# Kernel optimization log

Measured on AMD Instinct MI355X. Metric: run time of the kernel, lower is better.

The kernel has to match this reference:

```python
import jax, jax.numpy as jnp
import numpy as np


def setup_inputs() -> dict:
    key = jax.random.key(0)
    ks = jax.random.split(key, 8)
    B, C, T, F = 2, 2, 500, 129
    H, D = 16, 100  # hidden_channels, delay
    return {
        "x_mic": jax.random.normal(ks[0], (B, C, T, F), jnp.float32),
        "x_ref": jax.random.normal(ks[1], (B, C, T, F), jnp.float32),
        "w_mic": jax.random.normal(ks[2], (H, C), jnp.float32) * 0.5,
        "b_mic": jax.random.normal(ks[3], (H,), jnp.float32) * 0.1,
        "w_ref": jax.random.normal(ks[4], (H, C), jnp.float32) * 0.5,
        "b_ref": jax.random.normal(ks[5], (H,), jnp.float32) * 0.1,
        "w_conv": jax.random.normal(ks[6], (1, H, 5, 3), jnp.float32) * 0.05,
        "b_conv": jax.random.normal(ks[7], (1,), jnp.float32) * 0.1,
        "delay": D,
    }


def reference(x_mic, x_ref, w_mic, b_mic, w_ref, b_ref, w_conv, b_conv, delay):
    # x_mic, x_ref: (B, C, T, F)
    B, C, T, F = x_mic.shape
    # 1x1 convs == per-(t,f) channel mixing
    Q = jnp.einsum('bctf,hc->bhtf', x_mic, w_mic) + b_mic[None, :, None, None]
    K = jnp.einsum('bctf,hc->bhtf', x_ref, w_ref) + b_ref[None, :, None, None]

    # unfold: zero-pad (delay-1) frames at the start of T, take sliding windows
    # window index d at output frame t maps to K[t - (delay-1) + d]
    idx = jnp.arange(T)[:, None] + jnp.arange(delay)[None, :]  # (T, delay) indices into padded T
    Kp = jnp.pad(K, ((0, 0), (0, 0), (delay - 1, 0), (0, 0)))
    Ku = Kp[:, :, idx, :]  # (B, H, T, delay, F)

    # windowed cross-correlation over frequency
    V = jnp.einsum('bhtf,bhtdf->bhtd', Q, Ku)  # (B, H, T, delay)

    # (5,3) conv, causal pad 4 along T (height), symmetric pad 1 along delay (width)
    V = jax.lax.conv_general_dilated(
        V, w_conv, window_strides=(1, 1), padding=[(4, 0), (1, 1)],
        dimension_numbers=('NCHW', 'OIHW', 'NCHW'))
    V = V + b_conv[None, :, None, None]  # (B, 1, T, delay)

    A = jax.nn.softmax(V[:, 0], axis=-1)  # (B, T, delay) attention over delays

    # unfold raw x_ref the same way and take delay-weighted sum
    Rp = jnp.pad(x_ref, ((0, 0), (0, 0), (delay - 1, 0), (0, 0)))
    Ru = Rp[:, :, idx, :]  # (B, C, T, delay, F)
    y = jnp.einsum('bctdf,btd->bctf', Ru, A)  # (B, C, T, F)
    return y
```

## Files before the change

### kernel.cpp

```cpp
#include <hip/hip_runtime.h>
#include <math.h>

constexpr int NB = 2;
constexpr int NC = 2;
constexpr int NT = 500;
constexpr int NF = 129;
constexpr int NH = 16;
constexpr int ND = 100;

constexpr int NMAP = 9;
constexpr size_t CSTRIDE = (size_t)NT * ND;
constexpr size_t CELEMS  = (size_t)NB * NMAP * CSTRIDE;

typedef _Float16 f16;
typedef _Float16 f16x4 __attribute__((ext_vector_type(4)));
typedef float    f32x4 __attribute__((ext_vector_type(4)));

constexpr int TT    = 16;
constexpr int NTT   = 32;
constexpr int BROWS = 128;
constexpr int LROWS = 176;
constexpr int LSTR  = 148;

__global__ __launch_bounds__(256) void corr_kernel(
    const float* __restrict__ x_mic, const float* __restrict__ x_ref,
    float* __restrict__ C)
{
    __shared__ f16 Lds[LROWS * LSTR];

    const int tid = threadIdx.x;
    const int tt = blockIdx.x & 31;
    const int bj = blockIdx.x >> 5;
    const int j = bj % 3, b = bj / 3;
    const int ts = tt * TT;
    const int US = ts - (ND - 1);

    const float* xr = x_ref + (size_t)b * NC * NT * NF;
    const float* xm = x_mic + (size_t)b * NC * NT * NF;

    const int w = tid >> 6;
    const int l = tid & 63;

    for (int rr = 0; rr < 44; ++rr) {
        const int r = w + 4 * rr;
        f16* row = Lds + r * LSTR;
        float v0 = 0.f, v1 = 0.f, v2 = 0.f;
        if (r < BROWS) {
            const int u = US + r;
            if (u >= 0 && u < NT) {
                if (j < 2) {
                    const float* p = xr + (size_t)j * NT * NF + (size_t)u * NF;
                    v0 = p[l]; v1 = p[l + 64]; if (l == 0) v2 = p[128];
                } else { v0 = 1.f; v1 = 1.f; if (l == 0) v2 = 1.f; }
            }
        } else {
            const int q = r - BROWS;
            const int i = q >> 4;
            const int t = ts + (q & 15);
            if (t < NT) {
                if (i < 2) {
                    const float* p = xm + (size_t)i * NT * NF + (size_t)t * NF;
                    v0 = p[l]; v1 = p[l + 64]; if (l == 0) v2 = p[128];
                } else { v0 = 1.f; v1 = 1.f; if (l == 0) v2 = 1.f; }
            }
        }
        row[l]      = (f16)v0;
        row[l + 64] = (f16)v1;
        if (l < LSTR - 128) row[128 + l] = (l == 0) ? (f16)v2 : (f16)0.f;
    }
    __syncthreads();

    const int lr = l & 15;
    const int lk = l >> 4;
    f32x4 acc[3][2] = {};

    #pragma unroll
    for (int kk = 0; kk < 9; ++kk) {
        const int fo = 16 * kk + 4 * lk;
        f16x4 bf0 = *(const f16x4*)&Lds[(32*w      + lr) * LSTR + fo];
        f16x4 bf1 = *(const f16x4*)&Lds[(32*w + 16 + lr) * LSTR + fo];
        #pragma unroll
        for (int i = 0; i < 3; ++i) {
            f16x4 af = *(const f16x4*)&Lds[(BROWS + 16*i + lr) * LSTR + fo];
            acc[i][0] = __builtin_amdgcn_mfma_f32_16x16x16f16(af, bf0, acc[i][0], 0, 0, 0);
            acc[i][1] = __builtin_amdgcn_mfma_f32_16x16x16f16(af, bf1, acc[i][1], 0, 0, 0);
        }
    }

    #pragma unroll
    for (int i = 0; i < 3; ++i) {
        float* Cb = C + ((size_t)b * NMAP + (i*3 + j)) * CSTRIDE;
        #pragma unroll
        for (int n = 0; n < 2; ++n) {
            const int u_loc = 32*w + 16*n + lr;
            #pragma unroll
            for (int jj = 0; jj < 4; ++jj) {
                const int t_loc = 4*lk + jj;
                const int t_g = ts + t_loc;
                const int d = u_loc - t_loc;
                if (t_g < NT && d >= 0 && d < ND)
                    Cb[(size_t)t_g * ND + d] = acc[i][n][jj];
            }
        }
    }
}

__global__ __launch_bounds__(256) void csy_kernel(
    const float* __restrict__ C, const float* __restrict__ w_conv,
    const float* __restrict__ b_conv,
    const float* __restrict__ w_mic, const float* __restrict__ b_mic,
    const float* __restrict__ w_ref, const float* __restrict__ b_ref,
    const float* __restrict__ x_ref, float* __restrict__ y)
{
    const int t = blockIdx.x % NT;
    const int b = blockIdx.x / NT;
    const int tid = threadIdx.x;

    __shared__ float G[NMAP][15];
    __shared__ float Alds[ND];
    __shared__ float red[4];

    if (tid < NMAP * 15) {
        const int m = tid / 15, tap = tid % 15;
        const int i = m / 3, jj = m % 3;
        float s = 0.f;
        for (int h = 0; h < NH; ++h) {
            const float a  = (i  < 2) ? w_mic[h*NC + i]  : b_mic[h];
            const float bb = (jj < 2) ? w_ref[h*NC + jj] : b_ref[h];
            s += w_conv[h*15 + tap] * a * bb;
        }
        G[m][tap] = s;
    }
    __syncthreads();

    const int d = tid;
    float s = 0.f;
    if (d < ND) {
        const float* Cb = C + (size_t)b * NMAP * CSTRIDE;
        #pragma unroll
        for (int kt = 0; kt < 5; ++kt) {
            const int tp = t - 4 + kt;
            if (tp < 0) continue;
            #pragma unroll
            for (int kd = 0; kd < 3; ++kd) {
                const int dp = d - 1 + kd;
                if (dp < 0 || dp >= ND) continue;
                const float* p = Cb + (size_t)tp * ND + dp;
                const int tap = kt*3 + kd;
                float a2 = 0.f;
                #pragma unroll
                for (int m = 0; m < NMAP; ++m)
                    a2 += G[m][tap] * p[m * CSTRIDE];
                s += a2;
            }
        }
        s += b_conv[0];
    }

    if (tid < 128) {
        float mx = (d < ND) ? s : -3.4e38f;
        #pragma unroll
        for (int o = 32; o > 0; o >>= 1) mx = fmaxf(mx, __shfl_down(mx, o, 64));
        if ((tid & 63) == 0) red[tid >> 6] = mx;
    }
    __syncthreads();
    const float mx = fmaxf(red[0], red[1]);
    const float e = (d < ND) ? __expf(s - mx) : 0.f;
    if (tid < 128) {
        float sm = e;
        #pragma unroll
        for (int o = 32; o > 0; o >>= 1) sm += __shfl_down(sm, o, 64);
        if ((tid & 63) == 0) red[2 + (tid >> 6)] = sm;
    }
    __syncthreads();
    const float inv = 1.f / (red[2] + red[3]);
    if (d < ND) Alds[d] = e * inv;
    __syncthreads();

    const int d0 = (t >= ND - 1) ? 0 : (ND - 1 - t);
    for (int o = tid; o < NC * NF; o += 256) {
        const int c = o / NF, f = o - c * NF;
        const float* X = x_ref + ((size_t)(b*NC + c) * NT + (t + d0 - (ND - 1))) * NF + f;
        float acc = 0.f;
        #pragma unroll 4
        for (int dd = d0; dd < ND; ++dd) {
            acc += Alds[dd] * X[0];
            X += NF;
        }
        y[((size_t)(b*NC + c) * NT + t) * NF + f] = acc;
    }
}

extern "C" void kernel_launch(void* const* d_in, const int* in_sizes, int n_in,
                              void* d_out, int out_size, void* d_ws, size_t ws_size,
                              hipStream_t stream)
{
    const float* x_mic  = (const float*)d_in[0];
    const float* x_ref  = (const float*)d_in[1];
    const float* w_mic  = (const float*)d_in[2];
    const float* b_mic  = (const float*)d_in[3];
    const float* w_ref  = (const float*)d_in[4];
    const float* b_ref  = (const float*)d_in[5];
    const float* w_conv = (const float*)d_in[6];
    const float* b_conv = (const float*)d_in[7];
    float* y = (float*)d_out;

    float* C = (float*)d_ws;

    corr_kernel<<<dim3(NB * 3 * NTT), dim3(256), 0, stream>>>(x_mic, x_ref, C);
    csy_kernel<<<dim3(NB * NT), dim3(256), 0, stream>>>(
        C, w_conv, b_conv, w_mic, b_mic, w_ref, b_ref, x_ref, y);
}
```

Measured before the change: 108.5 us.

## Replace bias correlation maps with per-frame row sums

```diff
diff --git a/kernel.cpp b/kernel.cpp
--- a/kernel.cpp
+++ b/kernel.cpp
@@ -8,9 +8,9 @@
 constexpr int NH = 16;
 constexpr int ND = 100;
 
-constexpr int NMAP = 9;
 constexpr size_t CSTRIDE = (size_t)NT * ND;
-constexpr size_t CELEMS  = (size_t)NB * NMAP * CSTRIDE;
+constexpr size_t C4ELEMS = (size_t)NB * 4 * CSTRIDE;
+constexpr int RSRLEN = 600;
 
 typedef _Float16 f16;
 typedef _Float16 f16x4 __attribute__((ext_vector_type(4)));
@@ -19,19 +19,19 @@
 constexpr int TT    = 16;
 constexpr int NTT   = 32;
 constexpr int BROWS = 128;
-constexpr int LROWS = 176;
+constexpr int LROWS = 160;
 constexpr int LSTR  = 148;
 
 __global__ __launch_bounds__(256) void corr_kernel(
     const float* __restrict__ x_mic, const float* __restrict__ x_ref,
-    float* __restrict__ C)
+    float* __restrict__ C, float* __restrict__ rsm, float* __restrict__ rsr)
 {
     __shared__ f16 Lds[LROWS * LSTR];
 
     const int tid = threadIdx.x;
     const int tt = blockIdx.x & 31;
     const int bj = blockIdx.x >> 5;
-    const int j = bj % 3, b = bj / 3;
+    const int j = bj & 1, b = bj >> 1;
     const int ts = tt * TT;
     const int US = ts - (ND - 1);
 
@@ -41,27 +41,23 @@
     const int w = tid >> 6;
     const int l = tid & 63;
 
-    for (int rr = 0; rr < 44; ++rr) {
+    for (int rr = 0; rr < 40; ++rr) {
         const int r = w + 4 * rr;
         f16* row = Lds + r * LSTR;
         float v0 = 0.f, v1 = 0.f, v2 = 0.f;
         if (r < BROWS) {
             const int u = US + r;
             if (u >= 0 && u < NT) {
-                if (j < 2) {
-                    const float* p = xr + (size_t)j * NT * NF + (size_t)u * NF;
-                    v0 = p[l]; v1 = p[l + 64]; if (l == 0) v2 = p[128];
-                } else { v0 = 1.f; v1 = 1.f; if (l == 0) v2 = 1.f; }
+                const float* p = xr + (size_t)j * NT * NF + (size_t)u * NF;
+                v0 = p[l]; v1 = p[l + 64]; if (l == 0) v2 = p[128];
             }
         } else {
             const int q = r - BROWS;
             const int i = q >> 4;
             const int t = ts + (q & 15);
             if (t < NT) {
-                if (i < 2) {
-                    const float* p = xm + (size_t)i * NT * NF + (size_t)t * NF;
-                    v0 = p[l]; v1 = p[l + 64]; if (l == 0) v2 = p[128];
-                } else { v0 = 1.f; v1 = 1.f; if (l == 0) v2 = 1.f; }
+                const float* p = xm + (size_t)i * NT * NF + (size_t)t * NF;
+                v0 = p[l]; v1 = p[l + 64]; if (l == 0) v2 = p[128];
             }
         }
         row[l]      = (f16)v0;
@@ -72,7 +68,7 @@
 
     const int lr = l & 15;
     const int lk = l >> 4;
-    f32x4 acc[3][2] = {};
+    f32x4 acc[2][2] = {};
 
     #pragma unroll
     for (int kk = 0; kk < 9; ++kk) {
@@ -80,7 +76,7 @@
         f16x4 bf0 = *(const f16x4*)&Lds[(32*w      + lr) * LSTR + fo];
         f16x4 bf1 = *(const f16x4*)&Lds[(32*w + 16 + lr) * LSTR + fo];
         #pragma unroll
-        for (int i = 0; i < 3; ++i) {
+        for (int i = 0; i < 2; ++i) {
             f16x4 af = *(const f16x4*)&Lds[(BROWS + 16*i + lr) * LSTR + fo];
             acc[i][0] = __builtin_amdgcn_mfma_f32_16x16x16f16(af, bf0, acc[i][0], 0, 0, 0);
             acc[i][1] = __builtin_amdgcn_mfma_f32_16x16x16f16(af, bf1, acc[i][1], 0, 0, 0);
@@ -88,8 +84,8 @@
     }
 
     #pragma unroll
-    for (int i = 0; i < 3; ++i) {
-        float* Cb = C + ((size_t)b * NMAP + (i*3 + j)) * CSTRIDE;
+    for (int i = 0; i < 2; ++i) {
+        float* Cb = C + ((size_t)b * 4 + i*2 + j) * CSTRIDE;
         #pragma unroll
         for (int n = 0; n < 2; ++n) {
             const int u_loc = 32*w + 16*n + lr;
@@ -103,10 +99,40 @@
             }
         }
     }
+
+    #pragma unroll
+    for (int k = 0; k < 4; ++k) {
+        const int u = ts + 4*w + k;
+        if (u < NT) {
+            const float* p = xr + (size_t)j * NT * NF + (size_t)u * NF;
+            float v = p[l] + p[l + 64] + ((l == 0) ? p[128] : 0.f);
+            #pragma unroll
+            for (int o = 32; o > 0; o >>= 1) v += __shfl_down(v, o, 64);
+            if (l == 0) rsr[((size_t)b*2 + j) * RSRLEN + 99 + u] = v;
+        }
+    }
+    if (j == 0) {
+        #pragma unroll
+        for (int k = 0; k < 8; ++k) {
+            const int q = 8*w + k;
+            const int i = q >> 4;
+            const int t = ts + (q & 15);
+            if (t < NT) {
+                const float* p = xm + (size_t)i * NT * NF + (size_t)t * NF;
+                float v = p[l] + p[l + 64] + ((l == 0) ? p[128] : 0.f);
+                #pragma unroll
+                for (int o = 32; o > 0; o >>= 1) v += __shfl_down(v, o, 64);
+                if (l == 0) rsm[((size_t)b*2 + i) * NT + t] = v;
+            }
+        }
+    }
+    if (tt == 0 && tid < 99)
+        rsr[((size_t)b*2 + j) * RSRLEN + tid] = 0.f;
 }
 
 __global__ __launch_bounds__(256) void csy_kernel(
-    const float* __restrict__ C, const float* __restrict__ w_conv,
+    const float* __restrict__ C, const float* __restrict__ rsm,
+    const float* __restrict__ rsr, const float* __restrict__ w_conv,
     const float* __restrict__ b_conv,
     const float* __restrict__ w_mic, const float* __restrict__ b_mic,
     const float* __restrict__ w_ref, const float* __restrict__ b_ref,
@@ -116,11 +142,12 @@
     const int b = blockIdx.x / NT;
     const int tid = threadIdx.x;
 
-    __shared__ float G[NMAP][15];
+    __shared__ float G[9][15];
+    __shared__ float Bt[15];
     __shared__ float Alds[ND];
     __shared__ float red[4];
 
-    if (tid < NMAP * 15) {
+    if (tid < 9 * 15) {
         const int m = tid / 15, tap = tid % 15;
         const int i = m / 3, jj = m % 3;
         float s = 0.f;
@@ -133,10 +160,24 @@
     }
     __syncthreads();
 
+    if (tid < 15) {
+        const int kt = tid / 3;
+        const int tp = t - 4 + kt;
+        float v = 0.f;
+        if (tp >= 0)
+            v = G[8][tid] * (float)NF
+              + G[2][tid] * rsm[(size_t)(b*2 + 0) * NT + tp]
+              + G[5][tid] * rsm[(size_t)(b*2 + 1) * NT + tp];
+        Bt[tid] = v;
+    }
+    __syncthreads();
+
     const int d = tid;
     float s = 0.f;
     if (d < ND) {
-        const float* Cb = C + (size_t)b * NMAP * CSTRIDE;
+        const float* Cb   = C + (size_t)b * 4 * CSTRIDE;
+        const float* rsr0 = rsr + (size_t)b * 2 * RSRLEN;
+        const float* rsr1 = rsr0 + RSRLEN;
         #pragma unroll
         for (int kt = 0; kt < 5; ++kt) {
             const int tp = t - 4 + kt;
@@ -145,13 +186,15 @@
             for (int kd = 0; kd < 3; ++kd) {
                 const int dp = d - 1 + kd;
                 if (dp < 0 || dp >= ND) continue;
-                const float* p = Cb + (size_t)tp * ND + dp;
                 const int tap = kt*3 + kd;
-                float a2 = 0.f;
-                #pragma unroll
-                for (int m = 0; m < NMAP; ++m)
-                    a2 += G[m][tap] * p[m * CSTRIDE];
-                s += a2;
+                const size_t off = (size_t)tp * ND + dp;
+                float a2 = G[0][tap] * Cb[off]
+                         + G[1][tap] * Cb[CSTRIDE   + off]
+                         + G[3][tap] * Cb[2*CSTRIDE + off]
+                         + G[4][tap] * Cb[3*CSTRIDE + off];
+                const int ue = tp + dp;
+                a2 += G[6][tap] * rsr0[ue] + G[7][tap] * rsr1[ue];
+                s += a2 + ((ue >= 99) ? Bt[tap] : 0.f);
             }
         }
         s += b_conv[0];
@@ -205,9 +248,11 @@
     const float* b_conv = (const float*)d_in[7];
     float* y = (float*)d_out;
 
-    float* C = (float*)d_ws;
-
-    corr_kernel<<<dim3(NB * 3 * NTT), dim3(256), 0, stream>>>(x_mic, x_ref, C);
+    float* C   = (float*)d_ws;
+    float* rsm = C + C4ELEMS;
+    float* rsr = rsm + (size_t)NB * 2 * NT;
+
+    corr_kernel<<<dim3(NB * 2 * NTT), dim3(256), 0, stream>>>(x_mic, x_ref, C, rsm, rsr);
     csy_kernel<<<dim3(NB * NT), dim3(256), 0, stream>>>(
-        C, w_conv, b_conv, w_mic, b_mic, w_ref, b_ref, x_ref, y);
+        C, rsm, rsr, w_conv, b_conv, w_mic, b_mic, w_ref, b_ref, x_ref, y);
 }
```

New measurement: 109.9 us. Within noise of the previous version (+1.3%).
